# Performance work log

Hardware: AMD Instinct MI355X
Metric: run time of the kernel (lower is better)

## Reference

```python
import jax, jax.numpy as jnp
import numpy as np

B, L, T = 256, 512, 128


def setup_inputs() -> dict:
    key = jax.random.key(0)
    k1, k2, k3, k4, k5, k6 = jax.random.split(key, 6)
    inputs = jax.random.normal(k1, (B, L, T), dtype=jnp.float32)
    transitions = jax.random.normal(k2, (T, T), dtype=jnp.float32) * (2.0 / T) ** 0.5
    start_transitions = jax.random.normal(k3, (T,), dtype=jnp.float32)
    end_transitions = jax.random.normal(k4, (T,), dtype=jnp.float32)
    tags = jax.random.randint(k5, (B, L), 0, T, dtype=jnp.int32)
    lengths = jax.random.randint(k6, (B,), L // 2, L + 1, dtype=jnp.int32)
    mask = (jnp.arange(L)[None, :] < lengths[:, None]).astype(jnp.int32)
    return {"inputs": inputs, "transitions": transitions,
            "start_transitions": start_transitions, "end_transitions": end_transitions,
            "tags": tags, "mask": mask}


def _input_likelihood(logits, maskf, transitions, start_t, end_t):
    # logits [B,L,T], maskf [B,L] float
    alpha0 = start_t[None, :] + logits[:, 0]  # [B,T]

    def step(alpha, xs):
        emit, m = xs  # emit [B,T], m [B]
        inner = alpha[:, :, None] + emit[:, None, :] + transitions[None]  # [B,T,T]
        new_alpha = jax.nn.logsumexp(inner, axis=1)
        alpha = new_alpha * m[:, None] + alpha * (1.0 - m[:, None])
        return alpha, None

    xs = (jnp.swapaxes(logits[:, 1:], 0, 1), jnp.swapaxes(maskf[:, 1:], 0, 1))
    alpha, _ = jax.lax.scan(step, alpha0, xs)
    stops = alpha + end_t[None, :]
    return jax.nn.logsumexp(stops, axis=-1)  # [B]


def _joint_likelihood(logits, tags, maskf, transitions, start_t, end_t):
    b_idx = jnp.arange(logits.shape[0])
    score = start_t[tags[:, 0]]
    trans_scores = transitions[tags[:, :-1], tags[:, 1:]]  # [B,L-1]
    emit = jnp.take_along_axis(logits, tags[:, :, None], axis=2)[..., 0]  # [B,L]
    score = score + jnp.sum(trans_scores * maskf[:, 1:], axis=1)
    score = score + jnp.sum(emit[:, :-1] * maskf[:, :-1], axis=1)
    last_idx = jnp.sum(maskf, axis=1).astype(jnp.int32) - 1
    last_tags = tags[b_idx, last_idx]
    score = score + end_t[last_tags] + logits[:, -1][b_idx, last_tags] * maskf[:, -1]
    return score


def reference(inputs, transitions, start_transitions, end_transitions, tags, mask):
    maskf = mask.astype(inputs.dtype)
    log_den = _input_likelihood(inputs, maskf, transitions, start_transitions, end_transitions)
    log_num = _joint_likelihood(inputs, tags, maskf, transitions, start_transitions, end_transitions)
    return jnp.sum(log_num - log_den)
```

## Files before the change

kernel.cpp:

```cpp
#include <hip/hip_runtime.h>
#include <hip/hip_bf16.h>

#define BB 256
#define LL 512
#define TT 128
#define CH 16

typedef _Float16 h2 __attribute__((ext_vector_type(2)));
typedef unsigned int u32;

static __device__ inline h2 pkrtz(float a, float b) {
  return __builtin_bit_cast(h2, __builtin_amdgcn_cvt_pkrtz(a, b));
}

#if defined(__has_builtin)
#if __has_builtin(__builtin_amdgcn_fdot2)
#define FDOT2(a, b, c) __builtin_amdgcn_fdot2((a), (b), (c), false)
#endif
#endif
#ifndef FDOT2
static __device__ inline float fdot2_fb(h2 a, h2 b, float c) {
  return fmaf((float)a.x, (float)b.x, fmaf((float)a.y, (float)b.y, c));
}
#define FDOT2(a, b, c) fdot2_fb((a), (b), (c))
#endif

static __device__ inline float wave_max_dpp(float x) {
  int v = __float_as_int(x);
#define DPP_STEP(ctrl)                                                  \
  {                                                                     \
    int t = __builtin_amdgcn_update_dpp(v, v, (ctrl), 0xf, 0xf, false); \
    x = fmaxf(x, __int_as_float(t));                                    \
    v = __float_as_int(x);                                              \
  }
  DPP_STEP(0x111)
  DPP_STEP(0x112)
  DPP_STEP(0x114)
  DPP_STEP(0x118)
  DPP_STEP(0x142)
  DPP_STEP(0x143)
#undef DPP_STEP
  return __int_as_float(__builtin_amdgcn_readlane(v, 63));
}

__global__ __launch_bounds__(256)
__attribute__((amdgpu_waves_per_eu(1, 1)))
void crf_fb_kernel(const float* __restrict__ inputs,
                   const float* __restrict__ trans,
                   const float* __restrict__ start_t,
                   const float* __restrict__ end_t,
                   const int* __restrict__ tags,
                   const int* __restrict__ mask,
                   float* __restrict__ diff) {
  const int b = blockIdx.x;
  const int tid = threadIdx.x;
  const int lane = tid & 63;
  const int wid = tid >> 6;

  __shared__ __align__(16) float fbuf[2][CH * TT];
  __shared__ __align__(16) float bbuf[2][CH * TT];
  __shared__ __align__(16) h2 ef_lds[64];
  __shared__ __align__(16) h2 g_lds[64];
  __shared__ float numA_sh, numB_sh;
  __shared__ int sb_sh;

  int lm = 0;
  const int* mk = mask + b * LL;
#pragma unroll
  for (int q = 0; q < LL / 64; ++q) lm += mk[q * 64 + lane];
#pragma unroll
  for (int d = 1; d < 64; d <<= 1) lm += __shfl_xor(lm, d);
  const int len = lm;
  const int m = (len - 1) >> 1;
  const int NC = (len - 1 - m + CH - 1) / CH;

  const float* erow = inputs + (size_t)b * LL * TT;
  const float2* er2 = (const float2*)erow;
  const float2* tr2 = (const float2*)trans;

  auto STAGE = [&](float* dst, const float* gbase) {
    const uint4* gs = (const uint4*)gbase;
    uint4* ds = (uint4*)dst;
    uint4 v0 = gs[0 * 64 + lane], v1 = gs[1 * 64 + lane];
    uint4 v2 = gs[2 * 64 + lane], v3 = gs[3 * 64 + lane];
    uint4 v4 = gs[4 * 64 + lane], v5 = gs[5 * 64 + lane];
    uint4 v6 = gs[6 * 64 + lane], v7 = gs[7 * 64 + lane];
    ds[0 * 64 + lane] = v0;
    ds[1 * 64 + lane] = v1;
    ds[2 * 64 + lane] = v2;
    ds[3 * 64 + lane] = v3;
    ds[4 * 64 + lane] = v4;
    ds[5 * 64 + lane] = v5;
    ds[6 * 64 + lane] = v6;
    ds[7 * 64 + lane] = v7;
  };

  int S = 0;
  float inv_sc = 1.0f;
  int cur_ex = 0;
  h2 Ea0[64], Ea1[64];

  if (wid == 0) {
#pragma unroll
    for (int p = 0; p < 64; ++p) {
      float2 r0 = tr2[(2 * p) * 64 + lane];
      float2 r1 = tr2[(2 * p + 1) * 64 + lane];
      h2 c0, c1;
      c0.x = (_Float16)__expf(r0.x);
      c0.y = (_Float16)__expf(r1.x);
      c1.x = (_Float16)__expf(r0.y);
      c1.y = (_Float16)__expf(r1.y);
      Ea0[p] = c0;
      Ea1[p] = c1;
    }
    float2 em0 = er2[lane];
    float f0 = __expf(start_t[2 * lane] + em0.x);
    float f1 = __expf(start_t[2 * lane + 1] + em0.y);
    ef_lds[lane] = pkrtz(f0, f1);
    float mx = wave_max_dpp(fmaxf(f0, f1));
    int exm = (int)((__float_as_uint(mx) >> 23) & 255) - 127;
    inv_sc = __uint_as_float((unsigned)(120 - exm) << 23);
    cur_ex = exm + 7;
  } else if (wid == 1) {
#pragma unroll
    for (int p = 0; p < 64; ++p) {
      float2 r0 = tr2[(2 * lane) * 64 + p];
      float2 r1 = tr2[(2 * lane + 1) * 64 + p];
      h2 c0, c1;
      c0.x = (_Float16)__expf(r0.x);
      c0.y = (_Float16)__expf(r0.y);
      c1.x = (_Float16)__expf(r1.x);
      c1.y = (_Float16)__expf(r1.y);
      Ea0[p] = c0;
      Ea1[p] = c1;
    }
    float2 em = er2[(size_t)(len - 1) * 64 + lane];
    float g0 = __expf(end_t[2 * lane] + em.x);
    float g1 = __expf(end_t[2 * lane + 1] + em.y);
    g_lds[lane] = pkrtz(g0, g1);
    float mx = wave_max_dpp(fmaxf(g0, g1));
    int exm = (int)((__float_as_uint(mx) >> 23) & 255) - 127;
    inv_sc = __uint_as_float((unsigned)(120 - exm) << 23);
    cur_ex = exm + 7;
  } else if (wid == 2) {
    STAGE(fbuf[0], erow + 1 * TT);
    const int* tg = tags + (size_t)b * LL;
    const int hl = len >> 1;
    float sc = 0.f;
    for (int t = lane; t < hl; t += 64) {
      int cu = tg[t];
      sc += erow[(size_t)t * TT + cu];
      if (t >= 1) sc += trans[tg[t - 1] * TT + cu];
    }
    if (lane == 0) sc += start_t[tg[0]];
#pragma unroll
    for (int d = 1; d < 64; d <<= 1) sc += __shfl_xor(sc, d);
    if (lane == 0) numA_sh = sc;
  } else {
    STAGE(bbuf[0], erow + (size_t)(len - 1 - CH) * TT);
    const int* tg = tags + (size_t)b * LL;
    const int hl = len >> 1;
    float sc = 0.f;
    for (int t = hl + lane; t < len; t += 64) {
      int cu = tg[t];
      sc += erow[(size_t)t * TT + cu];
      sc += trans[tg[t - 1] * TT + cu];
    }
    if (lane == 0) sc += end_t[tg[len - 1]];
#pragma unroll
    for (int d = 1; d < 64; d <<= 1) sc += __shfl_xor(sc, d);
    if (lane == 0) numB_sh = sc;
  }

  __syncthreads();

  for (int c = 0; c < NC; ++c) {
    if (wid == 0) {
      const float2* emb = (const float2*)fbuf[c & 1];
      const int tbeg = 1 + CH * c;
      const int tend = min(tbeg + CH - 1, m);
      for (int t = tbeg; t <= tend; ++t) {
        float2 em = emb[(t - tbeg) * 64 + lane];
        float f0 = __expf(em.x) * inv_sc;
        float f1 = __expf(em.y) * inv_sc;
        float a0 = 0.f, a1 = 0.f, a2 = 0.f, a3 = 0.f;
        float c0 = 0.f, c1 = 0.f, c2 = 0.f, c3 = 0.f;
        const uint4* ep = (const uint4*)ef_lds;
#pragma unroll
        for (int r = 0; r < 16; ++r) {
          uint4 q = ep[r];
          h2 e0 = __builtin_bit_cast(h2, q.x);
          h2 e1 = __builtin_bit_cast(h2, q.y);
          h2 e2 = __builtin_bit_cast(h2, q.z);
          h2 e3 = __builtin_bit_cast(h2, q.w);
          a0 = FDOT2(e0, Ea0[4 * r + 0], a0);
          a1 = FDOT2(e1, Ea0[4 * r + 1], a1);
          a2 = FDOT2(e2, Ea0[4 * r + 2], a2);
          a3 = FDOT2(e3, Ea0[4 * r + 3], a3);
          c0 = FDOT2(e0, Ea1[4 * r + 0], c0);
          c1 = FDOT2(e1, Ea1[4 * r + 1], c1);
          c2 = FDOT2(e2, Ea1[4 * r + 2], c2);
          c3 = FDOT2(e3, Ea1[4 * r + 3], c3);
        }
        float w0 = ((a0 + a1) + (a2 + a3)) * f0;
        float w1 = ((c0 + c1) + (c2 + c3)) * f1;
        ef_lds[lane] = pkrtz(w0, w1);
        S += cur_ex;
        float mx = wave_max_dpp(fmaxf(w0, w1));
        int exm = (int)((__float_as_uint(mx) >> 23) & 255) - 127;
        inv_sc = __uint_as_float((unsigned)(120 - exm) << 23);
        cur_ex = exm + 7;
      }
    } else if (wid == 1) {
      const int thi = len - 2 - CH * c;
      const int lb = len - 1 - CH * (c + 1);
      const int tlo = max(m, lb);
      const float2* emb = (const float2*)bbuf[c & 1];
      for (int t = thi; t >= tlo; --t) {
        float2 em = emb[(t - lb) * 64 + lane];
        float pex0 = __expf(em.x);
        float pex1 = __expf(em.y);
        float a0 = 0.f, a1 = 0.f, a2 = 0.f, a3 = 0.f;
        float c0 = 0.f, c1 = 0.f, c2 = 0.f, c3 = 0.f;
        const uint4* gp = (const uint4*)g_lds;
#pragma unroll
        for (int r = 0; r < 16; ++r) {
          uint4 q = gp[r];
          h2 g0 = __builtin_bit_cast(h2, q.x);
          h2 g1 = __builtin_bit_cast(h2, q.y);
          h2 g2 = __builtin_bit_cast(h2, q.z);
          h2 g3 = __builtin_bit_cast(h2, q.w);
          a0 = FDOT2(g0, Ea0[4 * r + 0], a0);
          a1 = FDOT2(g1, Ea0[4 * r + 1], a1);
          a2 = FDOT2(g2, Ea0[4 * r + 2], a2);
          a3 = FDOT2(g3, Ea0[4 * r + 3], a3);
          c0 = FDOT2(g0, Ea1[4 * r + 0], c0);
          c1 = FDOT2(g1, Ea1[4 * r + 1], c1);
          c2 = FDOT2(g2, Ea1[4 * r + 2], c2);
          c3 = FDOT2(g3, Ea1[4 * r + 3], c3);
        }
        float v0 = (a0 + a1) + (a2 + a3);
        float v1 = (c0 + c1) + (c2 + c3);
        if (t > m) {
          v0 *= pex0;
          v1 *= pex1;
        }
        float w0 = v0 * inv_sc, w1 = v1 * inv_sc;
        g_lds[lane] = pkrtz(w0, w1);
        S += cur_ex;
        float mx = wave_max_dpp(fmaxf(w0, w1));
        int exm = (int)((__float_as_uint(mx) >> 23) & 255) - 127;
        inv_sc = __uint_as_float((unsigned)(120 - exm) << 23);
        cur_ex = exm + 7;
      }
    } else if (wid == 2) {
      if (c + 1 < NC) STAGE(fbuf[(c + 1) & 1], erow + (size_t)(1 + CH * (c + 1)) * TT);
    } else {
      if (c + 1 < NC) STAGE(bbuf[(c + 1) & 1], erow + (size_t)(len - 1 - CH * (c + 2)) * TT);
    }
    __syncthreads();
  }

  if (wid == 1 && lane == 0) sb_sh = S;
  __syncthreads();

  if (wid == 0) {
    h2 a = ef_lds[lane];
    h2 g = g_lds[lane];
    float v = (float)a.x * (float)g.x + (float)a.y * (float)g.y;
#pragma unroll
    for (int d = 1; d < 64; d <<= 1) v += __shfl_xor(v, d);
    if (lane == 0) {
      float log_den = (float)(S + sb_sh) * 0.6931471805599453f + __logf(v);
      diff[b] = (numA_sh + numB_sh) - log_den;
    }
  }
}

__global__ void crf_sum_kernel(const float* __restrict__ diff,
                               float* __restrict__ out) {
  const int tid = threadIdx.x;
  float v = diff[tid];
#pragma unroll
  for (int d = 1; d < 64; d <<= 1) v += __shfl_xor(v, d);
  __shared__ float r[4];
  if ((tid & 63) == 0) r[tid >> 6] = v;
  __syncthreads();
  if (tid == 0) out[0] = r[0] + r[1] + r[2] + r[3];
}

extern "C" void kernel_launch(void* const* d_in, const int* in_sizes, int n_in,
                              void* d_out, int out_size, void* d_ws, size_t ws_size,
                              hipStream_t stream) {
  const float* inputs = (const float*)d_in[0];
  const float* trans = (const float*)d_in[1];
  const float* start_t = (const float*)d_in[2];
  const float* end_t = (const float*)d_in[3];
  const int* tags = (const int*)d_in[4];
  const int* mask = (const int*)d_in[5];
  float* diff = (float*)d_ws;
  float* out = (float*)d_out;

  crf_fb_kernel<<<BB, 256, 0, stream>>>(inputs, trans, start_t, end_t, tags,
                                        mask, diff);
  crf_sum_kernel<<<1, 256, 0, stream>>>(diff, out);
}
```

Measured before the change: 128.1 us.

## Split each CRF direction across two waves and move numerator to separate blocks

The forward and backward recurrences now each use two waves, with each wave owning 64 of the 128 output tags. The per-step cross-wave max and state exchange go through double-buffered LDS slots and a lightweight barrier every step. Emission exponentials are now computed once during staging instead of inside the serial loop. The gold-path numerator moves to an extra set of 256 blocks, and waves_per_eu is relaxed so those blocks can co-reside. This halves the dot-product work on the critical path per step but adds a workgroup barrier on every timestep.

```diff
diff --git a/kernel.cpp b/kernel.cpp
--- a/kernel.cpp
+++ b/kernel.cpp
@@ -1,5 +1,4 @@
 #include <hip/hip_runtime.h>
-#include <hip/hip_bf16.h>
 
 #define BB 256
 #define LL 512
@@ -7,11 +6,6 @@
 #define CH 16
 
 typedef _Float16 h2 __attribute__((ext_vector_type(2)));
-typedef unsigned int u32;
-
-static __device__ inline h2 pkrtz(float a, float b) {
-  return __builtin_bit_cast(h2, __builtin_amdgcn_cvt_pkrtz(a, b));
-}
 
 #if defined(__has_builtin)
 #if __has_builtin(__builtin_amdgcn_fdot2)
@@ -33,36 +27,71 @@
     x = fmaxf(x, __int_as_float(t));                                    \
     v = __float_as_int(x);                                              \
   }
-  DPP_STEP(0x111)
-  DPP_STEP(0x112)
-  DPP_STEP(0x114)
-  DPP_STEP(0x118)
-  DPP_STEP(0x142)
-  DPP_STEP(0x143)
+  DPP_STEP(0x111) DPP_STEP(0x112) DPP_STEP(0x114) DPP_STEP(0x118)
+  DPP_STEP(0x142) DPP_STEP(0x143)
 #undef DPP_STEP
   return __int_as_float(__builtin_amdgcn_readlane(v, 63));
 }
 
+static __device__ inline void wg_bar() {
+  asm volatile("s_waitcnt lgkmcnt(0)\n\ts_barrier" ::: "memory");
+}
+
+static __device__ inline h2 bch2(unsigned u) { return __builtin_bit_cast(h2, u); }
+static __device__ inline unsigned expbits(unsigned u) {
+  return __float_as_uint(__expf(__uint_as_float(u)));
+}
+
 __global__ __launch_bounds__(256)
-__attribute__((amdgpu_waves_per_eu(1, 1)))
-void crf_fb_kernel(const float* __restrict__ inputs,
-                   const float* __restrict__ trans,
-                   const float* __restrict__ start_t,
-                   const float* __restrict__ end_t,
-                   const int* __restrict__ tags,
-                   const int* __restrict__ mask,
-                   float* __restrict__ diff) {
-  const int b = blockIdx.x;
+__attribute__((amdgpu_waves_per_eu(1, 2)))
+void crf_main(const float* __restrict__ inputs, const float* __restrict__ trans,
+              const float* __restrict__ start_t, const float* __restrict__ end_t,
+              const int* __restrict__ tags, const int* __restrict__ mask,
+              float* __restrict__ den, float* __restrict__ num) {
   const int tid = threadIdx.x;
   const int lane = tid & 63;
   const int wid = tid >> 6;
 
   __shared__ __align__(16) float fbuf[2][CH * TT];
   __shared__ __align__(16) float bbuf[2][CH * TT];
-  __shared__ __align__(16) h2 ef_lds[64];
-  __shared__ __align__(16) h2 g_lds[64];
-  __shared__ float numA_sh, numB_sh;
+  __shared__ __align__(16) h2 ef[2][64];
+  __shared__ __align__(16) h2 gb[2][64];
+  __shared__ __align__(16) float mslot[2][2][2];
+  __shared__ float npart[4];
   __shared__ int sb_sh;
+
+  if (blockIdx.x >= BB) {
+    const int b = blockIdx.x - BB;
+    int lm = 0;
+    const int* mk = mask + b * LL;
+#pragma unroll
+    for (int q = 0; q < LL / 64; ++q) lm += mk[q * 64 + lane];
+#pragma unroll
+    for (int d = 1; d < 64; d <<= 1) lm += __shfl_xor(lm, d);
+    const int len = lm;
+    const int* tg = tags + (size_t)b * LL;
+    const float* erow = inputs + (size_t)b * LL * TT;
+    const int lo = (wid * len) >> 2, hi = ((wid + 1) * len) >> 2;
+    float sc = 0.f;
+    for (int t = lo + lane; t < hi; t += 64) {
+      int cu = tg[t];
+      sc += erow[(size_t)t * TT + cu];
+      if (t >= 1) sc += trans[tg[t - 1] * TT + cu];
+    }
+#pragma unroll
+    for (int d = 1; d < 64; d <<= 1) sc += __shfl_xor(sc, d);
+    if (lane == 0) npart[wid] = sc;
+    __syncthreads();
+    if (tid == 0)
+      num[b] = npart[0] + npart[1] + npart[2] + npart[3] + start_t[tg[0]] +
+               end_t[tg[len - 1]];
+    return;
+  }
+
+  const int b = blockIdx.x;
+  const int dir = wid >> 1;
+  const int hw = wid & 1;
+  const int j = hw * 64 + lane;
 
   int lm = 0;
   const int* mk = mask + b * LL;
@@ -72,215 +101,154 @@
   for (int d = 1; d < 64; d <<= 1) lm += __shfl_xor(lm, d);
   const int len = lm;
   const int m = (len - 1) >> 1;
-  const int NC = (len - 1 - m + CH - 1) / CH;
+  const int K = len - 1 - m;
+  const int NC = (K + CH - 1) / CH;
 
   const float* erow = inputs + (size_t)b * LL * TT;
-  const float2* er2 = (const float2*)erow;
-  const float2* tr2 = (const float2*)trans;
-
-  auto STAGE = [&](float* dst, const float* gbase) {
+
+  uint4 st0, st1, st2, st3;
+  auto STLD = [&](const float* gbase) {
     const uint4* gs = (const uint4*)gbase;
-    uint4* ds = (uint4*)dst;
-    uint4 v0 = gs[0 * 64 + lane], v1 = gs[1 * 64 + lane];
-    uint4 v2 = gs[2 * 64 + lane], v3 = gs[3 * 64 + lane];
-    uint4 v4 = gs[4 * 64 + lane], v5 = gs[5 * 64 + lane];
-    uint4 v6 = gs[6 * 64 + lane], v7 = gs[7 * 64 + lane];
-    ds[0 * 64 + lane] = v0;
-    ds[1 * 64 + lane] = v1;
-    ds[2 * 64 + lane] = v2;
-    ds[3 * 64 + lane] = v3;
-    ds[4 * 64 + lane] = v4;
-    ds[5 * 64 + lane] = v5;
-    ds[6 * 64 + lane] = v6;
-    ds[7 * 64 + lane] = v7;
+    st0 = gs[0 * 64 + lane];
+    st1 = gs[1 * 64 + lane];
+    st2 = gs[2 * 64 + lane];
+    st3 = gs[3 * 64 + lane];
   };
+  auto STWR = [&](float* dstb) {
+    uint4* dst = (uint4*)(dstb + 8 * hw * TT);
+    uint4 o;
+    o.x = expbits(st0.x); o.y = expbits(st0.y); o.z = expbits(st0.z); o.w = expbits(st0.w);
+    dst[0 * 64 + lane] = o;
+    o.x = expbits(st1.x); o.y = expbits(st1.y); o.z = expbits(st1.z); o.w = expbits(st1.w);
+    dst[1 * 64 + lane] = o;
+    o.x = expbits(st2.x); o.y = expbits(st2.y); o.z = expbits(st2.z); o.w = expbits(st2.w);
+    dst[2 * 64 + lane] = o;
+    o.x = expbits(st3.x); o.y = expbits(st3.y); o.z = expbits(st3.z); o.w = expbits(st3.w);
+    dst[3 * 64 + lane] = o;
+  };
+
+  if (dir == 0) STLD(erow + (size_t)(1 + 8 * hw) * TT);
+  else          STLD(erow + (size_t)(len - 1 - CH + 8 * hw) * TT);
+
+  h2 E[64];
+  if (dir == 0) {
+#pragma unroll
+    for (int p = 0; p < 64; ++p) {
+      float t0 = trans[(2 * p) * TT + j];
+      float t1 = trans[(2 * p + 1) * TT + j];
+      h2 e;
+      e.x = (_Float16)__expf(t0);
+      e.y = (_Float16)__expf(t1);
+      E[p] = e;
+    }
+  } else {
+    const float2* tr2 = (const float2*)trans;
+#pragma unroll
+    for (int p = 0; p < 64; ++p) {
+      float2 r = tr2[j * 64 + p];
+      h2 e;
+      e.x = (_Float16)__expf(r.x);
+      e.y = (_Float16)__expf(r.y);
+      E[p] = e;
+    }
+  }
+
+  STWR(dir == 0 ? fbuf[0] : bbuf[0]);
 
   int S = 0;
-  float inv_sc = 1.0f;
-  int cur_ex = 0;
-  h2 Ea0[64], Ea1[64];
+  if (dir == 0) {
+    float f = __expf(start_t[j] + erow[j]);
+    ((_Float16*)ef[0])[j] = (_Float16)f;
+    float mx = wave_max_dpp(f);
+    if (lane == 0) mslot[0][0][hw] = mx;
+  } else {
+    float gv = __expf(end_t[j] + erow[(size_t)(len - 1) * TT + j]);
+    ((_Float16*)gb[0])[j] = (_Float16)gv;
+    float mx = wave_max_dpp(gv);
+    if (lane == 0) mslot[0][1][hw] = mx;
+  }
+  wg_bar();
+
+  auto DOTS = [&](const uint4* ep) -> float {
+    float a0 = 0.f, a1 = 0.f, a2 = 0.f, a3 = 0.f;
+#pragma unroll
+    for (int r = 0; r < 16; ++r) {
+      uint4 q = ep[r];
+      a0 = FDOT2(bch2(q.x), E[4 * r + 0], a0);
+      a1 = FDOT2(bch2(q.y), E[4 * r + 1], a1);
+      a2 = FDOT2(bch2(q.z), E[4 * r + 2], a2);
+      a3 = FDOT2(bch2(q.w), E[4 * r + 3], a3);
+    }
+    return (a0 + a1) + (a2 + a3);
+  };
+
+  for (int c = 0; c < NC; ++c) {
+    if (c + 1 < NC) {
+      if (dir == 0) STLD(erow + (size_t)(1 + CH * (c + 1) + 8 * hw) * TT);
+      else          STLD(erow + (size_t)(len - 1 - CH * (c + 2) + 8 * hw) * TT);
+    }
+    const int kend = min(CH * (c + 1), K);
+    const float* __restrict__ fb = fbuf[c & 1];
+    const float* __restrict__ bbm = bbuf[c & 1];
+#pragma unroll 1
+    for (int k = CH * c + 1; k <= kend; ++k) {
+      const int pr = (k - 1) & 1, pw = k & 1;
+      if (dir == 0) {
+        if (k <= m) {
+          float2 ms = *(const float2*)&mslot[pr][0][0];
+          float mx = fmaxf(ms.x, ms.y);
+          int exm = (int)((__float_as_uint(mx) >> 23) & 255) - 127;
+          float inv_sc = __uint_as_float((unsigned)(120 - exm) << 23);
+          S += exm + 7;
+          float v = DOTS((const uint4*)ef[pr]);
+          float femb = fb[(k - 1 - CH * c) * TT + j];
+          float w = v * (femb * inv_sc);
+          ((_Float16*)ef[pw])[j] = (_Float16)w;
+          float wm = wave_max_dpp(w);
+          if (lane == 0) mslot[pw][0][hw] = wm;
+        }
+      } else {
+        float2 ms = *(const float2*)&mslot[pr][1][0];
+        float mx = fmaxf(ms.x, ms.y);
+        int exm = (int)((__float_as_uint(mx) >> 23) & 255) - 127;
+        float inv_sc = __uint_as_float((unsigned)(120 - exm) << 23);
+        S += exm + 7;
+        float v = DOTS((const uint4*)gb[pr]);
+        float pex = bbm[(CH * (c + 1) - k) * TT + j];
+        if (len - 1 - k > m) v *= pex;
+        float w = v * inv_sc;
+        ((_Float16*)gb[pw])[j] = (_Float16)w;
+        float wm = wave_max_dpp(w);
+        if (lane == 0) mslot[pw][1][hw] = wm;
+      }
+      wg_bar();
+    }
+    if (c + 1 < NC) {
+      STWR(dir == 0 ? fbuf[(c + 1) & 1] : bbuf[(c + 1) & 1]);
+      wg_bar();
+    }
+  }
+
+  if (wid == 2 && lane == 0) sb_sh = S;
+  wg_bar();
 
   if (wid == 0) {
-#pragma unroll
-    for (int p = 0; p < 64; ++p) {
-      float2 r0 = tr2[(2 * p) * 64 + lane];
-      float2 r1 = tr2[(2 * p + 1) * 64 + lane];
-      h2 c0, c1;
-      c0.x = (_Float16)__expf(r0.x);
-      c0.y = (_Float16)__expf(r1.x);
-      c1.x = (_Float16)__expf(r0.y);
-      c1.y = (_Float16)__expf(r1.y);
-      Ea0[p] = c0;
-      Ea1[p] = c1;
-    }
-    float2 em0 = er2[lane];
-    float f0 = __expf(start_t[2 * lane] + em0.x);
-    float f1 = __expf(start_t[2 * lane + 1] + em0.y);
-    ef_lds[lane] = pkrtz(f0, f1);
-    float mx = wave_max_dpp(fmaxf(f0, f1));
-    int exm = (int)((__float_as_uint(mx) >> 23) & 255) - 127;
-    inv_sc = __uint_as_float((unsigned)(120 - exm) << 23);
-    cur_ex = exm + 7;
-  } else if (wid == 1) {
-#pragma unroll
-    for (int p = 0; p < 64; ++p) {
-      float2 r0 = tr2[(2 * lane) * 64 + p];
-      float2 r1 = tr2[(2 * lane + 1) * 64 + p];
-      h2 c0, c1;
-      c0.x = (_Float16)__expf(r0.x);
-      c0.y = (_Float16)__expf(r0.y);
-      c1.x = (_Float16)__expf(r1.x);
-      c1.y = (_Float16)__expf(r1.y);
-      Ea0[p] = c0;
-      Ea1[p] = c1;
-    }
-    float2 em = er2[(size_t)(len - 1) * 64 + lane];
-    float g0 = __expf(end_t[2 * lane] + em.x);
-    float g1 = __expf(end_t[2 * lane + 1] + em.y);
-    g_lds[lane] = pkrtz(g0, g1);
-    float mx = wave_max_dpp(fmaxf(g0, g1));
-    int exm = (int)((__float_as_uint(mx) >> 23) & 255) - 127;
-    inv_sc = __uint_as_float((unsigned)(120 - exm) << 23);
-    cur_ex = exm + 7;
-  } else if (wid == 2) {
-    STAGE(fbuf[0], erow + 1 * TT);
-    const int* tg = tags + (size_t)b * LL;
-    const int hl = len >> 1;
-    float sc = 0.f;
-    for (int t = lane; t < hl; t += 64) {
-      int cu = tg[t];
-      sc += erow[(size_t)t * TT + cu];
-      if (t >= 1) sc += trans[tg[t - 1] * TT + cu];
-    }
-    if (lane == 0) sc += start_t[tg[0]];
-#pragma unroll
-    for (int d = 1; d < 64; d <<= 1) sc += __shfl_xor(sc, d);
-    if (lane == 0) numA_sh = sc;
-  } else {
-    STAGE(bbuf[0], erow + (size_t)(len - 1 - CH) * TT);
-    const int* tg = tags + (size_t)b * LL;
-    const int hl = len >> 1;
-    float sc = 0.f;
-    for (int t = hl + lane; t < len; t += 64) {
-      int cu = tg[t];
-      sc += erow[(size_t)t * TT + cu];
-      sc += trans[tg[t - 1] * TT + cu];
-    }
-    if (lane == 0) sc += end_t[tg[len - 1]];
-#pragma unroll
-    for (int d = 1; d < 64; d <<= 1) sc += __shfl_xor(sc, d);
-    if (lane == 0) numB_sh = sc;
-  }
-
-  __syncthreads();
-
-  for (int c = 0; c < NC; ++c) {
-    if (wid == 0) {
-      const float2* emb = (const float2*)fbuf[c & 1];
-      const int tbeg = 1 + CH * c;
-      const int tend = min(tbeg + CH - 1, m);
-      for (int t = tbeg; t <= tend; ++t) {
-        float2 em = emb[(t - tbeg) * 64 + lane];
-        float f0 = __expf(em.x) * inv_sc;
-        float f1 = __expf(em.y) * inv_sc;
-        float a0 = 0.f, a1 = 0.f, a2 = 0.f, a3 = 0.f;
-        float c0 = 0.f, c1 = 0.f, c2 = 0.f, c3 = 0.f;
-        const uint4* ep = (const uint4*)ef_lds;
-#pragma unroll
-        for (int r = 0; r < 16; ++r) {
-          uint4 q = ep[r];
-          h2 e0 = __builtin_bit_cast(h2, q.x);
-          h2 e1 = __builtin_bit_cast(h2, q.y);
-          h2 e2 = __builtin_bit_cast(h2, q.z);
-          h2 e3 = __builtin_bit_cast(h2, q.w);
-          a0 = FDOT2(e0, Ea0[4 * r + 0], a0);
-          a1 = FDOT2(e1, Ea0[4 * r + 1], a1);
-          a2 = FDOT2(e2, Ea0[4 * r + 2], a2);
-          a3 = FDOT2(e3, Ea0[4 * r + 3], a3);
-          c0 = FDOT2(e0, Ea1[4 * r + 0], c0);
-          c1 = FDOT2(e1, Ea1[4 * r + 1], c1);
-          c2 = FDOT2(e2, Ea1[4 * r + 2], c2);
-          c3 = FDOT2(e3, Ea1[4 * r + 3], c3);
-        }
-        float w0 = ((a0 + a1) + (a2 + a3)) * f0;
-        float w1 = ((c0 + c1) + (c2 + c3)) * f1;
-        ef_lds[lane] = pkrtz(w0, w1);
-        S += cur_ex;
-        float mx = wave_max_dpp(fmaxf(w0, w1));
-        int exm = (int)((__float_as_uint(mx) >> 23) & 255) - 127;
-        inv_sc = __uint_as_float((unsigned)(120 - exm) << 23);
-        cur_ex = exm + 7;
-      }
-    } else if (wid == 1) {
-      const int thi = len - 2 - CH * c;
-      const int lb = len - 1 - CH * (c + 1);
-      const int tlo = max(m, lb);
-      const float2* emb = (const float2*)bbuf[c & 1];
-      for (int t = thi; t >= tlo; --t) {
-        float2 em = emb[(t - lb) * 64 + lane];
-        float pex0 = __expf(em.x);
-        float pex1 = __expf(em.y);
-        float a0 = 0.f, a1 = 0.f, a2 = 0.f, a3 = 0.f;
-        float c0 = 0.f, c1 = 0.f, c2 = 0.f, c3 = 0.f;
-        const uint4* gp = (const uint4*)g_lds;
-#pragma unroll
-        for (int r = 0; r < 16; ++r) {
-          uint4 q = gp[r];
-          h2 g0 = __builtin_bit_cast(h2, q.x);
-          h2 g1 = __builtin_bit_cast(h2, q.y);
-          h2 g2 = __builtin_bit_cast(h2, q.z);
-          h2 g3 = __builtin_bit_cast(h2, q.w);
-          a0 = FDOT2(g0, Ea0[4 * r + 0], a0);
-          a1 = FDOT2(g1, Ea0[4 * r + 1], a1);
-          a2 = FDOT2(g2, Ea0[4 * r + 2], a2);
-          a3 = FDOT2(g3, Ea0[4 * r + 3], a3);
-          c0 = FDOT2(g0, Ea1[4 * r + 0], c0);
-          c1 = FDOT2(g1, Ea1[4 * r + 1], c1);
-          c2 = FDOT2(g2, Ea1[4 * r + 2], c2);
-          c3 = FDOT2(g3, Ea1[4 * r + 3], c3);
-        }
-        float v0 = (a0 + a1) + (a2 + a3);
-        float v1 = (c0 + c1) + (c2 + c3);
-        if (t > m) {
-          v0 *= pex0;
-          v1 *= pex1;
-        }
-        float w0 = v0 * inv_sc, w1 = v1 * inv_sc;
-        g_lds[lane] = pkrtz(w0, w1);
-        S += cur_ex;
-        float mx = wave_max_dpp(fmaxf(w0, w1));
-        int exm = (int)((__float_as_uint(mx) >> 23) & 255) - 127;
-        inv_sc = __uint_as_float((unsigned)(120 - exm) << 23);
-        cur_ex = exm + 7;
-      }
-    } else if (wid == 2) {
-      if (c + 1 < NC) STAGE(fbuf[(c + 1) & 1], erow + (size_t)(1 + CH * (c + 1)) * TT);
-    } else {
-      if (c + 1 < NC) STAGE(bbuf[(c + 1) & 1], erow + (size_t)(len - 1 - CH * (c + 2)) * TT);
-    }
-    __syncthreads();
-  }
-
-  if (wid == 1 && lane == 0) sb_sh = S;
-  __syncthreads();
-
-  if (wid == 0) {
-    h2 a = ef_lds[lane];
-    h2 g = g_lds[lane];
-    float v = (float)a.x * (float)g.x + (float)a.y * (float)g.y;
+    const int pf = m & 1, pb = K & 1;
+    h2 a = ef[pf][lane];
+    h2 gg = gb[pb][lane];
+    float v = (float)a.x * (float)gg.x + (float)a.y * (float)gg.y;
 #pragma unroll
     for (int d = 1; d < 64; d <<= 1) v += __shfl_xor(v, d);
-    if (lane == 0) {
-      float log_den = (float)(S + sb_sh) * 0.6931471805599453f + __logf(v);
-      diff[b] = (numA_sh + numB_sh) - log_den;
-    }
-  }
-}
-
-__global__ void crf_sum_kernel(const float* __restrict__ diff,
+    if (lane == 0)
+      den[b] = (float)(S + sb_sh) * 0.6931471805599453f + __logf(v);
+  }
+}
+
+__global__ void crf_sum_kernel(const float* __restrict__ den,
+                               const float* __restrict__ num,
                                float* __restrict__ out) {
   const int tid = threadIdx.x;
-  float v = diff[tid];
+  float v = num[tid] - den[tid];
 #pragma unroll
   for (int d = 1; d < 64; d <<= 1) v += __shfl_xor(v, d);
   __shared__ float r[4];
@@ -298,10 +266,11 @@
   const float* end_t = (const float*)d_in[3];
   const int* tags = (const int*)d_in[4];
   const int* mask = (const int*)d_in[5];
-  float* diff = (float*)d_ws;
+  float* den = (float*)d_ws;
+  float* num = den + BB;
   float* out = (float*)d_out;
 
-  crf_fb_kernel<<<BB, 256, 0, stream>>>(inputs, trans, start_t, end_t, tags,
-                                        mask, diff);
-  crf_sum_kernel<<<1, 256, 0, stream>>>(diff, out);
-}
+  crf_main<<<2 * BB, 256, 0, stream>>>(inputs, trans, start_t, end_t, tags,
+                                       mask, den, num);
+  crf_sum_kernel<<<1, 256, 0, stream>>>(den, num, out);
+}
```

Result: slower. 155.7 us (+21.5%).

## Broadcast recurrence state via readlane into SGPRs and pre-exponentiate staged emissions

Applied to the files above, without the earlier changes.

The per-step state vector is no longer exchanged through LDS; each of 64 packed fp16 pairs is broadcast with readlane into scalar registers, which the dot-product loop then reads. The staging waves now apply exp to the emission rows while copying them into LDS, so the recurrence waves skip that exp. This removes the LDS write/read round trip and exp from the serial dependency chain, at the cost of 64 readlane instructions per step and higher scalar register pressure.

```diff
diff --git a/kernel.cpp b/kernel.cpp
--- a/kernel.cpp
+++ b/kernel.cpp
@@ -1,5 +1,4 @@
 #include <hip/hip_runtime.h>
-#include <hip/hip_bf16.h>
 
 #define BB 256
 #define LL 512
@@ -7,7 +6,6 @@
 #define CH 16
 
 typedef _Float16 h2 __attribute__((ext_vector_type(2)));
-typedef unsigned int u32;
 
 static __device__ inline h2 pkrtz(float a, float b) {
   return __builtin_bit_cast(h2, __builtin_amdgcn_cvt_pkrtz(a, b));
@@ -33,14 +31,15 @@
     x = fmaxf(x, __int_as_float(t));                                    \
     v = __float_as_int(x);                                              \
   }
-  DPP_STEP(0x111)
-  DPP_STEP(0x112)
-  DPP_STEP(0x114)
-  DPP_STEP(0x118)
-  DPP_STEP(0x142)
-  DPP_STEP(0x143)
+  DPP_STEP(0x111) DPP_STEP(0x112) DPP_STEP(0x114) DPP_STEP(0x118)
+  DPP_STEP(0x142) DPP_STEP(0x143)
 #undef DPP_STEP
   return __int_as_float(__builtin_amdgcn_readlane(v, 63));
+}
+
+static __device__ inline h2 bch2(unsigned u) { return __builtin_bit_cast(h2, u); }
+static __device__ inline unsigned expbits(unsigned u) {
+  return __float_as_uint(__expf(__uint_as_float(u)));
 }
 
 __global__ __launch_bounds__(256)
@@ -59,7 +58,6 @@
 
   __shared__ __align__(16) float fbuf[2][CH * TT];
   __shared__ __align__(16) float bbuf[2][CH * TT];
-  __shared__ __align__(16) h2 ef_lds[64];
   __shared__ __align__(16) h2 g_lds[64];
   __shared__ float numA_sh, numB_sh;
   __shared__ int sb_sh;
@@ -81,24 +79,26 @@
   auto STAGE = [&](float* dst, const float* gbase) {
     const uint4* gs = (const uint4*)gbase;
     uint4* ds = (uint4*)dst;
-    uint4 v0 = gs[0 * 64 + lane], v1 = gs[1 * 64 + lane];
-    uint4 v2 = gs[2 * 64 + lane], v3 = gs[3 * 64 + lane];
-    uint4 v4 = gs[4 * 64 + lane], v5 = gs[5 * 64 + lane];
-    uint4 v6 = gs[6 * 64 + lane], v7 = gs[7 * 64 + lane];
-    ds[0 * 64 + lane] = v0;
-    ds[1 * 64 + lane] = v1;
-    ds[2 * 64 + lane] = v2;
-    ds[3 * 64 + lane] = v3;
-    ds[4 * 64 + lane] = v4;
-    ds[5 * 64 + lane] = v5;
-    ds[6 * 64 + lane] = v6;
-    ds[7 * 64 + lane] = v7;
+    uint4 v[8];
+#pragma unroll
+    for (int q = 0; q < 8; ++q) v[q] = gs[q * 64 + lane];
+#pragma unroll
+    for (int q = 0; q < 8; ++q) {
+      uint4 o;
+      o.x = expbits(v[q].x);
+      o.y = expbits(v[q].y);
+      o.z = expbits(v[q].z);
+      o.w = expbits(v[q].w);
+      ds[q * 64 + lane] = o;
+    }
   };
 
   int S = 0;
   float inv_sc = 1.0f;
   int cur_ex = 0;
   h2 Ea0[64], Ea1[64];
+  unsigned sst[64];
+  h2 pk;
 
   if (wid == 0) {
 #pragma unroll
@@ -116,7 +116,11 @@
     float2 em0 = er2[lane];
     float f0 = __expf(start_t[2 * lane] + em0.x);
     float f1 = __expf(start_t[2 * lane + 1] + em0.y);
-    ef_lds[lane] = pkrtz(f0, f1);
+    pk = pkrtz(f0, f1);
+    int pki = (int)__builtin_bit_cast(unsigned, pk);
+#pragma unroll
+    for (int r = 0; r < 64; ++r)
+      sst[r] = (unsigned)__builtin_amdgcn_readlane(pki, r);
     float mx = wave_max_dpp(fmaxf(f0, f1));
     int exm = (int)((__float_as_uint(mx) >> 23) & 255) - 127;
     inv_sc = __uint_as_float((unsigned)(120 - exm) << 23);
@@ -137,7 +141,11 @@
     float2 em = er2[(size_t)(len - 1) * 64 + lane];
     float g0 = __expf(end_t[2 * lane] + em.x);
     float g1 = __expf(end_t[2 * lane + 1] + em.y);
-    g_lds[lane] = pkrtz(g0, g1);
+    pk = pkrtz(g0, g1);
+    int pki = (int)__builtin_bit_cast(unsigned, pk);
+#pragma unroll
+    for (int r = 0; r < 64; ++r)
+      sst[r] = (unsigned)__builtin_amdgcn_readlane(pki, r);
     float mx = wave_max_dpp(fmaxf(g0, g1));
     int exm = (int)((__float_as_uint(mx) >> 23) & 255) - 127;
     inv_sc = __uint_as_float((unsigned)(120 - exm) << 23);
@@ -179,32 +187,35 @@
       const float2* emb = (const float2*)fbuf[c & 1];
       const int tbeg = 1 + CH * c;
       const int tend = min(tbeg + CH - 1, m);
+#pragma unroll 1
       for (int t = tbeg; t <= tend; ++t) {
-        float2 em = emb[(t - tbeg) * 64 + lane];
-        float f0 = __expf(em.x) * inv_sc;
-        float f1 = __expf(em.y) * inv_sc;
+        float2 fe = emb[(t - tbeg) * 64 + lane];
+        float f0 = fe.x * inv_sc;
+        float f1 = fe.y * inv_sc;
         float a0 = 0.f, a1 = 0.f, a2 = 0.f, a3 = 0.f;
         float c0 = 0.f, c1 = 0.f, c2 = 0.f, c3 = 0.f;
-        const uint4* ep = (const uint4*)ef_lds;
-#pragma unroll
-        for (int r = 0; r < 16; ++r) {
-          uint4 q = ep[r];
-          h2 e0 = __builtin_bit_cast(h2, q.x);
-          h2 e1 = __builtin_bit_cast(h2, q.y);
-          h2 e2 = __builtin_bit_cast(h2, q.z);
-          h2 e3 = __builtin_bit_cast(h2, q.w);
-          a0 = FDOT2(e0, Ea0[4 * r + 0], a0);
-          a1 = FDOT2(e1, Ea0[4 * r + 1], a1);
-          a2 = FDOT2(e2, Ea0[4 * r + 2], a2);
-          a3 = FDOT2(e3, Ea0[4 * r + 3], a3);
-          c0 = FDOT2(e0, Ea1[4 * r + 0], c0);
-          c1 = FDOT2(e1, Ea1[4 * r + 1], c1);
-          c2 = FDOT2(e2, Ea1[4 * r + 2], c2);
-          c3 = FDOT2(e3, Ea1[4 * r + 3], c3);
+#pragma unroll
+        for (int q = 0; q < 16; ++q) {
+          h2 s0 = bch2(sst[4 * q + 0]);
+          h2 s1 = bch2(sst[4 * q + 1]);
+          h2 s2 = bch2(sst[4 * q + 2]);
+          h2 s3 = bch2(sst[4 * q + 3]);
+          a0 = FDOT2(s0, Ea0[4 * q + 0], a0);
+          a1 = FDOT2(s1, Ea0[4 * q + 1], a1);
+          a2 = FDOT2(s2, Ea0[4 * q + 2], a2);
+          a3 = FDOT2(s3, Ea0[4 * q + 3], a3);
+          c0 = FDOT2(s0, Ea1[4 * q + 0], c0);
+          c1 = FDOT2(s1, Ea1[4 * q + 1], c1);
+          c2 = FDOT2(s2, Ea1[4 * q + 2], c2);
+          c3 = FDOT2(s3, Ea1[4 * q + 3], c3);
         }
         float w0 = ((a0 + a1) + (a2 + a3)) * f0;
         float w1 = ((c0 + c1) + (c2 + c3)) * f1;
-        ef_lds[lane] = pkrtz(w0, w1);
+        pk = pkrtz(w0, w1);
+        int pki = (int)__builtin_bit_cast(unsigned, pk);
+#pragma unroll
+        for (int r = 0; r < 64; ++r)
+          sst[r] = (unsigned)__builtin_amdgcn_readlane(pki, r);
         S += cur_ex;
         float mx = wave_max_dpp(fmaxf(w0, w1));
         int exm = (int)((__float_as_uint(mx) >> 23) & 255) - 127;
@@ -216,37 +227,38 @@
       const int lb = len - 1 - CH * (c + 1);
       const int tlo = max(m, lb);
       const float2* emb = (const float2*)bbuf[c & 1];
+#pragma unroll 1
       for (int t = thi; t >= tlo; --t) {
-        float2 em = emb[(t - lb) * 64 + lane];
-        float pex0 = __expf(em.x);
-        float pex1 = __expf(em.y);
+        float2 pe = emb[(t - lb) * 64 + lane];
         float a0 = 0.f, a1 = 0.f, a2 = 0.f, a3 = 0.f;
         float c0 = 0.f, c1 = 0.f, c2 = 0.f, c3 = 0.f;
-        const uint4* gp = (const uint4*)g_lds;
-#pragma unroll
-        for (int r = 0; r < 16; ++r) {
-          uint4 q = gp[r];
-          h2 g0 = __builtin_bit_cast(h2, q.x);
-          h2 g1 = __builtin_bit_cast(h2, q.y);
-          h2 g2 = __builtin_bit_cast(h2, q.z);
-          h2 g3 = __builtin_bit_cast(h2, q.w);
-          a0 = FDOT2(g0, Ea0[4 * r + 0], a0);
-          a1 = FDOT2(g1, Ea0[4 * r + 1], a1);
-          a2 = FDOT2(g2, Ea0[4 * r + 2], a2);
-          a3 = FDOT2(g3, Ea0[4 * r + 3], a3);
-          c0 = FDOT2(g0, Ea1[4 * r + 0], c0);
-          c1 = FDOT2(g1, Ea1[4 * r + 1], c1);
-          c2 = FDOT2(g2, Ea1[4 * r + 2], c2);
-          c3 = FDOT2(g3, Ea1[4 * r + 3], c3);
+#pragma unroll
+        for (int q = 0; q < 16; ++q) {
+          h2 s0 = bch2(sst[4 * q + 0]);
+          h2 s1 = bch2(sst[4 * q + 1]);
+          h2 s2 = bch2(sst[4 * q + 2]);
+          h2 s3 = bch2(sst[4 * q + 3]);
+          a0 = FDOT2(s0, Ea0[4 * q + 0], a0);
+          a1 = FDOT2(s1, Ea0[4 * q + 1], a1);
+          a2 = FDOT2(s2, Ea0[4 * q + 2], a2);
+          a3 = FDOT2(s3, Ea0[4 * q + 3], a3);
+          c0 = FDOT2(s0, Ea1[4 * q + 0], c0);
+          c1 = FDOT2(s1, Ea1[4 * q + 1], c1);
+          c2 = FDOT2(s2, Ea1[4 * q + 2], c2);
+          c3 = FDOT2(s3, Ea1[4 * q + 3], c3);
         }
         float v0 = (a0 + a1) + (a2 + a3);
         float v1 = (c0 + c1) + (c2 + c3);
         if (t > m) {
-          v0 *= pex0;
-          v1 *= pex1;
+          v0 *= pe.x;
+          v1 *= pe.y;
         }
         float w0 = v0 * inv_sc, w1 = v1 * inv_sc;
-        g_lds[lane] = pkrtz(w0, w1);
+        pk = pkrtz(w0, w1);
+        int pki = (int)__builtin_bit_cast(unsigned, pk);
+#pragma unroll
+        for (int r = 0; r < 64; ++r)
+          sst[r] = (unsigned)__builtin_amdgcn_readlane(pki, r);
         S += cur_ex;
         float mx = wave_max_dpp(fmaxf(w0, w1));
         int exm = (int)((__float_as_uint(mx) >> 23) & 255) - 127;
@@ -261,11 +273,14 @@
     __syncthreads();
   }
 
-  if (wid == 1 && lane == 0) sb_sh = S;
+  if (wid == 1) {
+    g_lds[lane] = pk;
+    if (lane == 0) sb_sh = S;
+  }
   __syncthreads();
 
   if (wid == 0) {
-    h2 a = ef_lds[lane];
+    h2 a = pk;
     h2 g = g_lds[lane];
     float v = (float)a.x * (float)g.x + (float)a.y * (float)g.y;
 #pragma unroll
```

Result: slower. 167.3 us (+30.5%).

## Drop LDS staging waves; prefetch emissions into registers with 4-deep rolling loads

Applied to the files above, without the earlier changes.

Removes the two producer waves that staged emission chunks into LDS double buffers and the per-chunk block barriers. The forward and backward waves now load their own emissions straight from global memory, keeping four steps of prefetch in registers, and they also compute the numerator halves. The block shrinks to 128 threads and needs only one final barrier. This avoids chunk-level synchronisation stalls and the LDS round-trip, but global load latency must now be covered by the 4-step prefetch.

```diff
diff --git a/kernel.cpp b/kernel.cpp
--- a/kernel.cpp
+++ b/kernel.cpp
@@ -1,13 +1,10 @@
 #include <hip/hip_runtime.h>
-#include <hip/hip_bf16.h>
 
 #define BB 256
 #define LL 512
 #define TT 128
-#define CH 16
 
 typedef _Float16 h2 __attribute__((ext_vector_type(2)));
-typedef unsigned int u32;
 
 static __device__ inline h2 pkrtz(float a, float b) {
   return __builtin_bit_cast(h2, __builtin_amdgcn_cvt_pkrtz(a, b));
@@ -33,17 +30,15 @@
     x = fmaxf(x, __int_as_float(t));                                    \
     v = __float_as_int(x);                                              \
   }
-  DPP_STEP(0x111)
-  DPP_STEP(0x112)
-  DPP_STEP(0x114)
-  DPP_STEP(0x118)
-  DPP_STEP(0x142)
-  DPP_STEP(0x143)
+  DPP_STEP(0x111) DPP_STEP(0x112) DPP_STEP(0x114) DPP_STEP(0x118)
+  DPP_STEP(0x142) DPP_STEP(0x143)
 #undef DPP_STEP
   return __int_as_float(__builtin_amdgcn_readlane(v, 63));
 }
 
-__global__ __launch_bounds__(256)
+static __device__ inline h2 bch2(unsigned u) { return __builtin_bit_cast(h2, u); }
+
+__global__ __launch_bounds__(128)
 __attribute__((amdgpu_waves_per_eu(1, 1)))
 void crf_fb_kernel(const float* __restrict__ inputs,
                    const float* __restrict__ trans,
@@ -57,8 +52,6 @@
   const int lane = tid & 63;
   const int wid = tid >> 6;
 
-  __shared__ __align__(16) float fbuf[2][CH * TT];
-  __shared__ __align__(16) float bbuf[2][CH * TT];
   __shared__ __align__(16) h2 ef_lds[64];
   __shared__ __align__(16) h2 g_lds[64];
   __shared__ float numA_sh, numB_sh;
@@ -72,35 +65,33 @@
   for (int d = 1; d < 64; d <<= 1) lm += __shfl_xor(lm, d);
   const int len = lm;
   const int m = (len - 1) >> 1;
-  const int NC = (len - 1 - m + CH - 1) / CH;
 
   const float* erow = inputs + (size_t)b * LL * TT;
   const float2* er2 = (const float2*)erow;
+  const float2* esrc = er2 + lane;
   const float2* tr2 = (const float2*)trans;
-
-  auto STAGE = [&](float* dst, const float* gbase) {
-    const uint4* gs = (const uint4*)gbase;
-    uint4* ds = (uint4*)dst;
-    uint4 v0 = gs[0 * 64 + lane], v1 = gs[1 * 64 + lane];
-    uint4 v2 = gs[2 * 64 + lane], v3 = gs[3 * 64 + lane];
-    uint4 v4 = gs[4 * 64 + lane], v5 = gs[5 * 64 + lane];
-    uint4 v6 = gs[6 * 64 + lane], v7 = gs[7 * 64 + lane];
-    ds[0 * 64 + lane] = v0;
-    ds[1 * 64 + lane] = v1;
-    ds[2 * 64 + lane] = v2;
-    ds[3 * 64 + lane] = v3;
-    ds[4 * 64 + lane] = v4;
-    ds[5 * 64 + lane] = v5;
-    ds[6 * 64 + lane] = v6;
-    ds[7 * 64 + lane] = v7;
-  };
 
   int S = 0;
   float inv_sc = 1.0f;
   int cur_ex = 0;
   h2 Ea0[64], Ea1[64];
+  h2 pk;
 
   if (wid == 0) {
+    {
+      const int* tg = tags + (size_t)b * LL;
+      const int hl = len >> 1;
+      float sc = 0.f;
+      for (int t = lane; t < hl; t += 64) {
+        int cu = tg[t];
+        sc += erow[(size_t)t * TT + cu];
+        if (t >= 1) sc += trans[tg[t - 1] * TT + cu];
+      }
+      if (lane == 0) sc += start_t[tg[0]];
+#pragma unroll
+      for (int d = 1; d < 64; d <<= 1) sc += __shfl_xor(sc, d);
+      if (lane == 0) numA_sh = sc;
+    }
 #pragma unroll
     for (int p = 0; p < 64; ++p) {
       float2 r0 = tr2[(2 * p) * 64 + lane];
@@ -113,15 +104,72 @@
       Ea0[p] = c0;
       Ea1[p] = c1;
     }
-    float2 em0 = er2[lane];
+    float2 em0 = esrc[0];
     float f0 = __expf(start_t[2 * lane] + em0.x);
     float f1 = __expf(start_t[2 * lane + 1] + em0.y);
-    ef_lds[lane] = pkrtz(f0, f1);
+    pk = pkrtz(f0, f1);
+    ef_lds[lane] = pk;
     float mx = wave_max_dpp(fmaxf(f0, f1));
     int exm = (int)((__float_as_uint(mx) >> 23) & 255) - 127;
     inv_sc = __uint_as_float((unsigned)(120 - exm) << 23);
     cur_ex = exm + 7;
-  } else if (wid == 1) {
+
+    const uint4* ep = (const uint4*)ef_lds;
+    auto FSTEP = [&](float2 fe) {
+      float ff0 = __expf(fe.x) * inv_sc;
+      float ff1 = __expf(fe.y) * inv_sc;
+      float a0 = 0.f, a1 = 0.f, a2 = 0.f, a3 = 0.f;
+      float c0 = 0.f, c1 = 0.f, c2 = 0.f, c3 = 0.f;
+#pragma unroll
+      for (int r = 0; r < 16; ++r) {
+        uint4 q = ep[r];
+        h2 e0 = bch2(q.x), e1 = bch2(q.y), e2 = bch2(q.z), e3 = bch2(q.w);
+        a0 = FDOT2(e0, Ea0[4 * r + 0], a0);
+        a1 = FDOT2(e1, Ea0[4 * r + 1], a1);
+        a2 = FDOT2(e2, Ea0[4 * r + 2], a2);
+        a3 = FDOT2(e3, Ea0[4 * r + 3], a3);
+        c0 = FDOT2(e0, Ea1[4 * r + 0], c0);
+        c1 = FDOT2(e1, Ea1[4 * r + 1], c1);
+        c2 = FDOT2(e2, Ea1[4 * r + 2], c2);
+        c3 = FDOT2(e3, Ea1[4 * r + 3], c3);
+      }
+      float w0 = ((a0 + a1) + (a2 + a3)) * ff0;
+      float w1 = ((c0 + c1) + (c2 + c3)) * ff1;
+      pk = pkrtz(w0, w1);
+      ef_lds[lane] = pk;
+      S += cur_ex;
+      float mx2 = wave_max_dpp(fmaxf(w0, w1));
+      int ex2 = (int)((__float_as_uint(mx2) >> 23) & 255) - 127;
+      inv_sc = __uint_as_float((unsigned)(120 - ex2) << 23);
+      cur_ex = ex2 + 7;
+    };
+    float2 feA = esrc[1 * 64], feB = esrc[2 * 64];
+    float2 feC = esrc[3 * 64], feD = esrc[4 * 64];
+    int t = 1;
+    for (; t + 3 <= m; t += 4) {
+      FSTEP(feA); feA = esrc[(size_t)(t + 4) * 64];
+      FSTEP(feB); feB = esrc[(size_t)(t + 5) * 64];
+      FSTEP(feC); feC = esrc[(size_t)(t + 6) * 64];
+      FSTEP(feD); feD = esrc[(size_t)(t + 7) * 64];
+    }
+    if (t <= m) { FSTEP(feA); ++t; }
+    if (t <= m) { FSTEP(feB); ++t; }
+    if (t <= m) { FSTEP(feC); ++t; }
+  } else {
+    {
+      const int* tg = tags + (size_t)b * LL;
+      const int hl = len >> 1;
+      float sc = 0.f;
+      for (int t = hl + lane; t < len; t += 64) {
+        int cu = tg[t];
+        sc += erow[(size_t)t * TT + cu];
+        sc += trans[tg[t - 1] * TT + cu];
+      }
+      if (lane == 0) sc += end_t[tg[len - 1]];
+#pragma unroll
+      for (int d = 1; d < 64; d <<= 1) sc += __shfl_xor(sc, d);
+      if (lane == 0) numB_sh = sc;
+    }
 #pragma unroll
     for (int p = 0; p < 64; ++p) {
       float2 r0 = tr2[(2 * lane) * 64 + p];
@@ -134,138 +182,69 @@
       Ea0[p] = c0;
       Ea1[p] = c1;
     }
-    float2 em = er2[(size_t)(len - 1) * 64 + lane];
+    float2 em = esrc[(size_t)(len - 1) * 64];
     float g0 = __expf(end_t[2 * lane] + em.x);
     float g1 = __expf(end_t[2 * lane + 1] + em.y);
-    g_lds[lane] = pkrtz(g0, g1);
+    pk = pkrtz(g0, g1);
+    g_lds[lane] = pk;
     float mx = wave_max_dpp(fmaxf(g0, g1));
     int exm = (int)((__float_as_uint(mx) >> 23) & 255) - 127;
     inv_sc = __uint_as_float((unsigned)(120 - exm) << 23);
     cur_ex = exm + 7;
-  } else if (wid == 2) {
-    STAGE(fbuf[0], erow + 1 * TT);
-    const int* tg = tags + (size_t)b * LL;
-    const int hl = len >> 1;
-    float sc = 0.f;
-    for (int t = lane; t < hl; t += 64) {
-      int cu = tg[t];
-      sc += erow[(size_t)t * TT + cu];
-      if (t >= 1) sc += trans[tg[t - 1] * TT + cu];
-    }
-    if (lane == 0) sc += start_t[tg[0]];
-#pragma unroll
-    for (int d = 1; d < 64; d <<= 1) sc += __shfl_xor(sc, d);
-    if (lane == 0) numA_sh = sc;
-  } else {
-    STAGE(bbuf[0], erow + (size_t)(len - 1 - CH) * TT);
-    const int* tg = tags + (size_t)b * LL;
-    const int hl = len >> 1;
-    float sc = 0.f;
-    for (int t = hl + lane; t < len; t += 64) {
-      int cu = tg[t];
-      sc += erow[(size_t)t * TT + cu];
-      sc += trans[tg[t - 1] * TT + cu];
-    }
-    if (lane == 0) sc += end_t[tg[len - 1]];
-#pragma unroll
-    for (int d = 1; d < 64; d <<= 1) sc += __shfl_xor(sc, d);
-    if (lane == 0) numB_sh = sc;
+
+    const uint4* gp = (const uint4*)g_lds;
+    auto BSTEP = [&](float2 pe, int tt) {
+      float pex0 = __expf(pe.x);
+      float pex1 = __expf(pe.y);
+      float a0 = 0.f, a1 = 0.f, a2 = 0.f, a3 = 0.f;
+      float c0 = 0.f, c1 = 0.f, c2 = 0.f, c3 = 0.f;
+#pragma unroll
+      for (int r = 0; r < 16; ++r) {
+        uint4 q = gp[r];
+        h2 e0 = bch2(q.x), e1 = bch2(q.y), e2 = bch2(q.z), e3 = bch2(q.w);
+        a0 = FDOT2(e0, Ea0[4 * r + 0], a0);
+        a1 = FDOT2(e1, Ea0[4 * r + 1], a1);
+        a2 = FDOT2(e2, Ea0[4 * r + 2], a2);
+        a3 = FDOT2(e3, Ea0[4 * r + 3], a3);
+        c0 = FDOT2(e0, Ea1[4 * r + 0], c0);
+        c1 = FDOT2(e1, Ea1[4 * r + 1], c1);
+        c2 = FDOT2(e2, Ea1[4 * r + 2], c2);
+        c3 = FDOT2(e3, Ea1[4 * r + 3], c3);
+      }
+      float v0 = (a0 + a1) + (a2 + a3);
+      float v1 = (c0 + c1) + (c2 + c3);
+      if (tt > m) {
+        v0 *= pex0;
+        v1 *= pex1;
+      }
+      float w0 = v0 * inv_sc, w1 = v1 * inv_sc;
+      pk = pkrtz(w0, w1);
+      g_lds[lane] = pk;
+      S += cur_ex;
+      float mx2 = wave_max_dpp(fmaxf(w0, w1));
+      int ex2 = (int)((__float_as_uint(mx2) >> 23) & 255) - 127;
+      inv_sc = __uint_as_float((unsigned)(120 - ex2) << 23);
+      cur_ex = ex2 + 7;
+    };
+    float2 feA = esrc[(size_t)(len - 2) * 64], feB = esrc[(size_t)(len - 3) * 64];
+    float2 feC = esrc[(size_t)(len - 4) * 64], feD = esrc[(size_t)(len - 5) * 64];
+    int t = len - 2;
+    for (; t - 3 >= m; t -= 4) {
+      BSTEP(feA, t);     feA = esrc[(size_t)(t - 4) * 64];
+      BSTEP(feB, t - 1); feB = esrc[(size_t)(t - 5) * 64];
+      BSTEP(feC, t - 2); feC = esrc[(size_t)(t - 6) * 64];
+      BSTEP(feD, t - 3); feD = esrc[(size_t)(t - 7) * 64];
+    }
+    if (t >= m) { BSTEP(feA, t); --t; }
+    if (t >= m) { BSTEP(feB, t); --t; }
+    if (t >= m) { BSTEP(feC, t); --t; }
+    if (lane == 0) sb_sh = S;
   }
 
   __syncthreads();
 
-  for (int c = 0; c < NC; ++c) {
-    if (wid == 0) {
-      const float2* emb = (const float2*)fbuf[c & 1];
-      const int tbeg = 1 + CH * c;
-      const int tend = min(tbeg + CH - 1, m);
-      for (int t = tbeg; t <= tend; ++t) {
-        float2 em = emb[(t - tbeg) * 64 + lane];
-        float f0 = __expf(em.x) * inv_sc;
-        float f1 = __expf(em.y) * inv_sc;
-        float a0 = 0.f, a1 = 0.f, a2 = 0.f, a3 = 0.f;
-        float c0 = 0.f, c1 = 0.f, c2 = 0.f, c3 = 0.f;
-        const uint4* ep = (const uint4*)ef_lds;
-#pragma unroll
-        for (int r = 0; r < 16; ++r) {
-          uint4 q = ep[r];
-          h2 e0 = __builtin_bit_cast(h2, q.x);
-          h2 e1 = __builtin_bit_cast(h2, q.y);
-          h2 e2 = __builtin_bit_cast(h2, q.z);
-          h2 e3 = __builtin_bit_cast(h2, q.w);
-          a0 = FDOT2(e0, Ea0[4 * r + 0], a0);
-          a1 = FDOT2(e1, Ea0[4 * r + 1], a1);
-          a2 = FDOT2(e2, Ea0[4 * r + 2], a2);
-          a3 = FDOT2(e3, Ea0[4 * r + 3], a3);
-          c0 = FDOT2(e0, Ea1[4 * r + 0], c0);
-          c1 = FDOT2(e1, Ea1[4 * r + 1], c1);
-          c2 = FDOT2(e2, Ea1[4 * r + 2], c2);
-          c3 = FDOT2(e3, Ea1[4 * r + 3], c3);
-        }
-        float w0 = ((a0 + a1) + (a2 + a3)) * f0;
-        float w1 = ((c0 + c1) + (c2 + c3)) * f1;
-        ef_lds[lane] = pkrtz(w0, w1);
-        S += cur_ex;
-        float mx = wave_max_dpp(fmaxf(w0, w1));
-        int exm = (int)((__float_as_uint(mx) >> 23) & 255) - 127;
-        inv_sc = __uint_as_float((unsigned)(120 - exm) << 23);
-        cur_ex = exm + 7;
-      }
-    } else if (wid == 1) {
-      const int thi = len - 2 - CH * c;
-      const int lb = len - 1 - CH * (c + 1);
-      const int tlo = max(m, lb);
-      const float2* emb = (const float2*)bbuf[c & 1];
-      for (int t = thi; t >= tlo; --t) {
-        float2 em = emb[(t - lb) * 64 + lane];
-        float pex0 = __expf(em.x);
-        float pex1 = __expf(em.y);
-        float a0 = 0.f, a1 = 0.f, a2 = 0.f, a3 = 0.f;
-        float c0 = 0.f, c1 = 0.f, c2 = 0.f, c3 = 0.f;
-        const uint4* gp = (const uint4*)g_lds;
-#pragma unroll
-        for (int r = 0; r < 16; ++r) {
-          uint4 q = gp[r];
-          h2 g0 = __builtin_bit_cast(h2, q.x);
-          h2 g1 = __builtin_bit_cast(h2, q.y);
-          h2 g2 = __builtin_bit_cast(h2, q.z);
-          h2 g3 = __builtin_bit_cast(h2, q.w);
-          a0 = FDOT2(g0, Ea0[4 * r + 0], a0);
-          a1 = FDOT2(g1, Ea0[4 * r + 1], a1);
-          a2 = FDOT2(g2, Ea0[4 * r + 2], a2);
-          a3 = FDOT2(g3, Ea0[4 * r + 3], a3);
-          c0 = FDOT2(g0, Ea1[4 * r + 0], c0);
-          c1 = FDOT2(g1, Ea1[4 * r + 1], c1);
-          c2 = FDOT2(g2, Ea1[4 * r + 2], c2);
-          c3 = FDOT2(g3, Ea1[4 * r + 3], c3);
-        }
-        float v0 = (a0 + a1) + (a2 + a3);
-        float v1 = (c0 + c1) + (c2 + c3);
-        if (t > m) {
-          v0 *= pex0;
-          v1 *= pex1;
-        }
-        float w0 = v0 * inv_sc, w1 = v1 * inv_sc;
-        g_lds[lane] = pkrtz(w0, w1);
-        S += cur_ex;
-        float mx = wave_max_dpp(fmaxf(w0, w1));
-        int exm = (int)((__float_as_uint(mx) >> 23) & 255) - 127;
-        inv_sc = __uint_as_float((unsigned)(120 - exm) << 23);
-        cur_ex = exm + 7;
-      }
-    } else if (wid == 2) {
-      if (c + 1 < NC) STAGE(fbuf[(c + 1) & 1], erow + (size_t)(1 + CH * (c + 1)) * TT);
-    } else {
-      if (c + 1 < NC) STAGE(bbuf[(c + 1) & 1], erow + (size_t)(len - 1 - CH * (c + 2)) * TT);
-    }
-    __syncthreads();
-  }
-
-  if (wid == 1 && lane == 0) sb_sh = S;
-  __syncthreads();
-
   if (wid == 0) {
-    h2 a = ef_lds[lane];
+    h2 a = pk;
     h2 g = g_lds[lane];
     float v = (float)a.x * (float)g.x + (float)a.y * (float)g.y;
 #pragma unroll
@@ -301,7 +280,7 @@
   float* diff = (float*)d_ws;
   float* out = (float*)d_out;
 
-  crf_fb_kernel<<<BB, 256, 0, stream>>>(inputs, trans, start_t, end_t, tags,
+  crf_fb_kernel<<<BB, 128, 0, stream>>>(inputs, trans, start_t, end_t, tags,
                                         mask, diff);
   crf_sum_kernel<<<1, 256, 0, stream>>>(diff, out);
 }
```

Result: slower. 184.7 us (+44.1%).
